# Kernel tuning notes

Measured on AMD Instinct MI355X. Metric: run time of the kernel, lower is better.

Reference implementation:

```python
import jax, jax.numpy as jnp
import numpy as np

BLOCK = 128          # quantization block size (K-blocks for activations, 128x128 for weight)
FP8_MAX = 448.0      # max normal of float8_e4m3fn


def _quant_weight(w):
    """Block-quantize a [N, K] weight to fp8 values (stored in f32) + [N/128, K/128] scales."""
    N, K = w.shape
    wb = w.reshape(N // BLOCK, BLOCK, K // BLOCK, BLOCK)
    ws = jnp.max(jnp.abs(wb), axis=(1, 3)) / FP8_MAX          # [N/128, K/128]
    ws_full = jnp.repeat(jnp.repeat(ws, BLOCK, axis=0), BLOCK, axis=1)  # [N, K]
    w_fp8 = (w / ws_full).astype(jnp.float8_e4m3fn).astype(jnp.float32)
    return w_fp8, ws


def setup_inputs() -> dict:
    key = jax.random.key(0)
    k1, k2 = jax.random.split(key)
    x = jax.random.normal(k1, (4, 2048, 4096), dtype=jnp.float32)
    w = jax.random.normal(k2, (4096, 4096), dtype=jnp.float32) * 0.02
    weight, weight_scale = _quant_weight(w)
    return {"x": x, "weight": weight, "weight_scale": weight_scale}


def reference(x, weight, weight_scale):
    """FP8Linear forward: dynamic per-128-block activation quant + scaled fp8 GEMM.

    x:            [..., K] float32
    weight:       [N, K]   fp8 values stored as float32
    weight_scale: [N/128, K/128] float32 per-block weight scales
    """
    *lead, K = x.shape
    N = weight.shape[0]
    # --- act_quant: per-row, per-128-K-block dynamic scale, round-trip through fp8 ---
    xb = x.reshape(-1, K // BLOCK, BLOCK)                      # [M, Kb, 128]
    s = jnp.max(jnp.abs(xb), axis=-1, keepdims=True) / FP8_MAX # [M, Kb, 1]
    xq = (xb / s).astype(jnp.float8_e4m3fn).astype(jnp.float32)
    a = (xq * s).reshape(-1, K)                                # dequantized activations [M, K]
    # --- fp8_gemm: per-block dequant folds into the accumulation; since scales are
    # constant within each K-block, this equals a plain GEMM of dequantized operands ---
    ws_full = jnp.repeat(jnp.repeat(weight_scale, BLOCK, axis=0), BLOCK, axis=1)  # [N, K]
    w_deq = weight * ws_full
    y = a @ w_deq.T                                            # [M, N] fp32 accumulate
    return y.reshape(*lead, N)
```

## Files before the change

### kernel.cpp

```cpp
#include <hip/hip_runtime.h>
#include <hip/hip_fp8.h>
#include <stdint.h>

#define K_DIM 4096
#define N_DIM 4096
#define NKB   32

using f32x4 = __attribute__((ext_vector_type(4))) float;
using i32x4 = __attribute__((ext_vector_type(4))) int;
using i32x8 = __attribute__((ext_vector_type(8))) int;

#define GLOAD_LDS16(g, l)                                                      \
    __builtin_amdgcn_global_load_lds(                                          \
        (const __attribute__((address_space(1))) unsigned int*)(g),            \
        (__attribute__((address_space(3))) unsigned int*)(l), 16, 0, 0)
#define GLOAD_LDS4(g, l)                                                       \
    __builtin_amdgcn_global_load_lds(                                          \
        (const __attribute__((address_space(1))) unsigned int*)(g),            \
        (__attribute__((address_space(3))) unsigned int*)(l), 4, 0, 0)

__device__ __forceinline__ uint8_t to_fp8(float v) {
    __hip_fp8_e4m3 q(v);
    return (uint8_t)q.__x;
}

__global__ __launch_bounds__(256) void act_quant_kernel(
    const float* __restrict__ x, uint8_t* __restrict__ xq,
    float* __restrict__ saT, int M)
{
    int gw   = blockIdx.x * 4 + (threadIdx.x >> 6);
    int lane = threadIdx.x & 63;
    int m    = gw >> 5;
    int kb   = gw & 31;
    size_t base = (size_t)m * K_DIM + kb * 128 + lane * 2;
    float2 v = *(const float2*)(x + base);
    float amax = fmaxf(fabsf(v.x), fabsf(v.y));
    #pragma unroll
    for (int o = 32; o >= 1; o >>= 1) amax = fmaxf(amax, __shfl_xor(amax, o));
    float s = amax / 448.0f;
    uchar2 q;
    q.x = to_fp8(v.x / s);
    q.y = to_fp8(v.y / s);
    *(uchar2*)(xq + base) = q;
    if (lane == 0) saT[(size_t)kb * M + m] = s;
}

__global__ __launch_bounds__(256) void w_quant_kernel(
    const float* __restrict__ w, uint8_t* __restrict__ wq)
{
    size_t i = ((size_t)blockIdx.x * 256 + threadIdx.x) * 4;
    float4 v = *(const float4*)(w + i);
    uchar4 q;
    q.x = to_fp8(v.x); q.y = to_fp8(v.y); q.z = to_fp8(v.z); q.w = to_fp8(v.w);
    *(uchar4*)(wq + i) = q;
}

#define LSA(b) ((b) * 66560)
#define LSB(b) ((b) * 66560 + 32768)
#define LSS(b) ((b) * 66560 + 65536)

__global__ __launch_bounds__(512, 1) void fp8_gemm_mx4(
    const uint8_t* __restrict__ Aq, const uint8_t* __restrict__ Bq,
    const float* __restrict__ saT, const float* __restrict__ wscale,
    float* __restrict__ C, int M)
{
    __shared__ __align__(16) uint8_t lds[133120];

    const int t    = threadIdx.x;
    const int lane = t & 63;
    const int lr   = lane & 15;
    const int lk   = lane >> 4;
    const int wid  = t >> 6;
    const int wm   = wid >> 2;
    const int wn   = wid & 3;

    const int gridN = N_DIM / 256;
    int nwg = (M / 256) * gridN;
    int cpx = nwg >> 3;
    int bid = blockIdx.x;
    int swz = (bid & 7) * cpx + (bid >> 3);
    const int m0 = (swz / gridN) * 256;
    const int n0 = (swz % gridN) * 256;
    const int nbI = ((n0 >> 7) + (wn >> 1)) * NKB;

    const int srow = t >> 3;
    const int scol = ((t & 7) ^ (srow & 7)) * 16;
    const uint8_t* gA = Aq + (size_t)(m0 + srow) * K_DIM + scol;
    const uint8_t* gB = Bq + (size_t)(n0 + srow) * K_DIM + scol;
    const int ldst = t * 16;

    const int fsw = (lr & 7) << 4;
    const int c0  = (lk * 32) ^ fsw;

#define STAGE(buf, kbi) do {                                                   \
    size_t ko_ = (size_t)(kbi) * 128;                                          \
    _Pragma("unroll") for (int j = 0; j < 4; ++j) {                            \
        GLOAD_LDS16(gA + ko_ + (size_t)j * 64 * K_DIM,                         \
                    &lds[LSA(buf) + j * 8192 + ldst]);                         \
        GLOAD_LDS16(gB + ko_ + (size_t)j * 64 * K_DIM,                         \
                    &lds[LSB(buf) + j * 8192 + ldst]);                         \
    }                                                                          \
    if (wid < 4)                                                               \
        GLOAD_LDS4(saT + (size_t)(kbi) * M + m0 + wid * 64 + lane,             \
                   &lds[LSS(buf) + wid * 256 + lane * 4]);                     \
} while (0)

    f32x4 acc[8][4] = {};
    const f32x4 vzero = {0.f, 0.f, 0.f, 0.f};

    STAGE(0, 0);
    asm volatile("s_waitcnt vmcnt(0)" ::: "memory");
    __builtin_amdgcn_s_barrier();

    #pragma unroll 2
    for (int kb = 0; kb < NKB; ++kb) {
        const int cur = kb & 1;
        if (kb < NKB - 1) STAGE(cur ^ 1, kb + 1);

        const int aB = LSA(cur), bB = LSB(cur), sB = LSS(cur);
        const float rw = wscale[nbI + kb];

        i32x8 bf[4];
        #pragma unroll
        for (int ni = 0; ni < 4; ++ni) {
            int rb = bB + (wn * 64 + ni * 16 + lr) * 128;
            i32x4 lo = *(const i32x4*)&lds[rb + c0];
            i32x4 hi = *(const i32x4*)&lds[rb + (c0 ^ 16)];
            bf[ni] = __builtin_shufflevector(lo, hi, 0, 1, 2, 3, 4, 5, 6, 7);
        }
        #pragma unroll
        for (int mh = 0; mh < 2; ++mh) {
            i32x8 af[4];
            #pragma unroll
            for (int mi = 0; mi < 4; ++mi) {
                int rb = aB + (wm * 128 + mh * 64 + mi * 16 + lr) * 128;
                i32x4 lo = *(const i32x4*)&lds[rb + c0];
                i32x4 hi = *(const i32x4*)&lds[rb + (c0 ^ 16)];
                af[mi] = __builtin_shufflevector(lo, hi, 0, 1, 2, 3, 4, 5, 6, 7);
            }
            #pragma unroll
            for (int mi = 0; mi < 4; ++mi) {
                f32x4 s4 = *(const f32x4*)&lds[sB + (wm * 128 + mh * 64 + mi * 16 + lk * 4) * 4];
                f32x4 sc = s4 * rw;
                f32x4 bs[4];
                #pragma unroll
                for (int ni = 0; ni < 4; ++ni)
                    bs[ni] = __builtin_amdgcn_mfma_scale_f32_16x16x128_f8f6f4(
                        af[mi], bf[ni], vzero, 0, 0,
                        0, 0x7F7F7F7F, 0, 0x7F7F7F7F);
                #pragma unroll
                for (int ni = 0; ni < 4; ++ni)
                    acc[mh * 4 + mi][ni] += bs[ni] * sc;
            }
        }

        asm volatile("s_waitcnt vmcnt(0)" ::: "memory");
        __builtin_amdgcn_s_barrier();
    }
#undef STAGE

    #pragma unroll
    for (int q = 0; q < 8; ++q) {
        int mh = q >> 2, mi = q & 3;
        #pragma unroll
        for (int j = 0; j < 4; ++j) {
            int m = m0 + wm * 128 + mh * 64 + mi * 16 + lk * 4 + j;
            float* crow = C + (size_t)m * N_DIM + n0 + wn * 64;
            #pragma unroll
            for (int ni = 0; ni < 4; ++ni)
                crow[ni * 16 + lr] = acc[q][ni][j];
        }
    }
}

extern "C" void kernel_launch(void* const* d_in, const int* in_sizes, int n_in,
                              void* d_out, int out_size, void* d_ws, size_t ws_size,
                              hipStream_t stream) {
    const float* x      = (const float*)d_in[0];
    const float* w      = (const float*)d_in[1];
    const float* wscale = (const float*)d_in[2];
    float* out = (float*)d_out;
    int M = in_sizes[0] / K_DIM;

    uint8_t* xq  = (uint8_t*)d_ws;
    uint8_t* wq  = xq + (size_t)M * K_DIM;
    float*   saT = (float*)(wq + (size_t)N_DIM * K_DIM);

    act_quant_kernel<<<M * NKB / 4, 256, 0, stream>>>(x, xq, saT, M);
    w_quant_kernel<<<((size_t)N_DIM * K_DIM) / 1024, 256, 0, stream>>>(w, wq);

    int nwg = (M / 256) * (N_DIM / 256);
    fp8_gemm_mx4<<<nwg, 512, 0, stream>>>(xq, wq, saT, wscale, out, M);
}
```

Baseline: 234.5 us.

## Accumulate MFMA in place using rescaling by consecutive block scale ratios

Replaces the per-K-block pattern of a zero-initialized MFMA followed by a scaled add with an in-place MFMA accumulate. The accumulator is first rescaled by the ratio of the previous block's scales to the current block's scales, and the final block's scales are applied in the epilogue. A new small kernel precomputes the activation and weight scale ratios. This removes the separate FMA pass after each MFMA and the temporary result registers. In exchange it adds a kernel launch and a multiply per accumulator per block, and it risks precision loss, or inf/NaN if a block scale is zero.

```diff
diff --git a/kernel.cpp b/kernel.cpp
--- a/kernel.cpp
+++ b/kernel.cpp
@@ -55,13 +55,33 @@
     *(uchar4*)(wq + i) = q;
 }
 
+__global__ __launch_bounds__(256) void ratio_kernel(
+    const float* __restrict__ saT, const float* __restrict__ ws,
+    float* __restrict__ ra, float* __restrict__ rwr, int M)
+{
+    int idx = blockIdx.x * 256 + threadIdx.x;
+    if (idx < 32 * M) {
+        int sb = idx / M, m = idx - sb * M;
+        float v = 1.0f;
+        if (sb >= 1) v = saT[(size_t)(sb - 1) * M + m] / saT[(size_t)sb * M + m];
+        ra[idx] = v;
+    }
+    if (idx < 32 * 32) {
+        int sb = idx >> 5, nb = idx & 31;
+        float v = 1.0f;
+        if (sb >= 1) v = ws[nb * NKB + sb - 1] / ws[nb * NKB + sb];
+        rwr[idx] = v;
+    }
+}
+
 #define LSA(b) ((b) * 66560)
 #define LSB(b) ((b) * 66560 + 32768)
 #define LSS(b) ((b) * 66560 + 65536)
 
-__global__ __launch_bounds__(512, 1) void fp8_gemm_mx4(
+__global__ __launch_bounds__(512, 1) void fp8_gemm_mx9(
     const uint8_t* __restrict__ Aq, const uint8_t* __restrict__ Bq,
-    const float* __restrict__ saT, const float* __restrict__ wscale,
+    const float* __restrict__ saT, const float* __restrict__ ra,
+    const float* __restrict__ rwr, const float* __restrict__ wscale,
     float* __restrict__ C, int M)
 {
     __shared__ __align__(16) uint8_t lds[133120];
@@ -81,7 +101,7 @@
     int swz = (bid & 7) * cpx + (bid >> 3);
     const int m0 = (swz / gridN) * 256;
     const int n0 = (swz % gridN) * 256;
-    const int nbI = ((n0 >> 7) + (wn >> 1)) * NKB;
+    const int nb = (n0 >> 7) + (wn >> 1);
 
     const int srow = t >> 3;
     const int scol = ((t & 7) ^ (srow & 7)) * 16;
@@ -101,12 +121,11 @@
                     &lds[LSB(buf) + j * 8192 + ldst]);                         \
     }                                                                          \
     if (wid < 4)                                                               \
-        GLOAD_LDS4(saT + (size_t)(kbi) * M + m0 + wid * 64 + lane,             \
+        GLOAD_LDS4(ra + (size_t)(kbi) * M + m0 + wid * 64 + lane,              \
                    &lds[LSS(buf) + wid * 256 + lane * 4]);                     \
 } while (0)
 
     f32x4 acc[8][4] = {};
-    const f32x4 vzero = {0.f, 0.f, 0.f, 0.f};
 
     STAGE(0, 0);
     asm volatile("s_waitcnt vmcnt(0)" ::: "memory");
@@ -118,7 +137,7 @@
         if (kb < NKB - 1) STAGE(cur ^ 1, kb + 1);
 
         const int aB = LSA(cur), bB = LSB(cur), sB = LSS(cur);
-        const float rw = wscale[nbI + kb];
+        const float rwc = rwr[kb * 32 + nb];
 
         i32x8 bf[4];
         #pragma unroll
@@ -140,17 +159,17 @@
             }
             #pragma unroll
             for (int mi = 0; mi < 4; ++mi) {
-                f32x4 s4 = *(const f32x4*)&lds[sB + (wm * 128 + mh * 64 + mi * 16 + lk * 4) * 4];
-                f32x4 sc = s4 * rw;
-                f32x4 bs[4];
+                f32x4 ra4 = *(const f32x4*)&lds[sB + (wm * 128 + mh * 64 + mi * 16 + lk * 4) * 4];
+                f32x4 sc = ra4 * rwc;
                 #pragma unroll
                 for (int ni = 0; ni < 4; ++ni)
-                    bs[ni] = __builtin_amdgcn_mfma_scale_f32_16x16x128_f8f6f4(
-                        af[mi], bf[ni], vzero, 0, 0,
-                        0, 0x7F7F7F7F, 0, 0x7F7F7F7F);
+                    acc[mh * 4 + mi][ni] *= sc;
                 #pragma unroll
                 for (int ni = 0; ni < 4; ++ni)
-                    acc[mh * 4 + mi][ni] += bs[ni] * sc;
+                    acc[mh * 4 + mi][ni] =
+                        __builtin_amdgcn_mfma_scale_f32_16x16x128_f8f6f4(
+                            af[mi], bf[ni], acc[mh * 4 + mi][ni],
+                            0, 0, 0, 0x7F7F7F7F, 0, 0x7F7F7F7F);
             }
         }
 
@@ -159,16 +178,19 @@
     }
 #undef STAGE
 
+    const float ws31 = wscale[nb * NKB + 31];
     #pragma unroll
     for (int q = 0; q < 8; ++q) {
         int mh = q >> 2, mi = q & 3;
+        f32x4 s31 = *(const f32x4*)(saT + (size_t)31 * M + m0 + wm * 128 + mh * 64 + mi * 16 + lk * 4);
+        f32x4 sc = s31 * ws31;
         #pragma unroll
         for (int j = 0; j < 4; ++j) {
             int m = m0 + wm * 128 + mh * 64 + mi * 16 + lk * 4 + j;
             float* crow = C + (size_t)m * N_DIM + n0 + wn * 64;
             #pragma unroll
             for (int ni = 0; ni < 4; ++ni)
-                crow[ni * 16 + lr] = acc[q][ni][j];
+                crow[ni * 16 + lr] = acc[q][ni][j] * sc[j];
         }
     }
 }
@@ -185,10 +207,13 @@
     uint8_t* xq  = (uint8_t*)d_ws;
     uint8_t* wq  = xq + (size_t)M * K_DIM;
     float*   saT = (float*)(wq + (size_t)N_DIM * K_DIM);
+    float*   ra  = saT + (size_t)NKB * M;
+    float*   rwr = ra + (size_t)NKB * M;
 
     act_quant_kernel<<<M * NKB / 4, 256, 0, stream>>>(x, xq, saT, M);
     w_quant_kernel<<<((size_t)N_DIM * K_DIM) / 1024, 256, 0, stream>>>(w, wq);
+    ratio_kernel<<<(32 * M + 255) / 256, 256, 0, stream>>>(saT, wscale, ra, rwr, M);
 
     int nwg = (M / 256) * (N_DIM / 256);
-    fp8_gemm_mx4<<<nwg, 512, 0, stream>>>(xq, wq, saT, wscale, out, M);
-}
+    fp8_gemm_mx9<<<nwg, 512, 0, stream>>>(xq, wq, saT, ra, rwr, wscale, out, M);
+}
```

Result: no change. 236.1 us (+0.7%).
